# Optimization experiments

Hardware: AMD Instinct MI355X
Metric: run time of the kernel (lower is better)

## Reference

```python
import jax, jax.numpy as jnp
import numpy as np
from jax import lax

B, C_IN, C_OUT, H, W, K, MID = 16, 256, 256, 64, 64, 3, 64
BN_EPS = 1e-5


def setup_inputs() -> dict:
    key = jax.random.key(0)
    ks = jax.random.split(key, 16)
    inp = {
        'x': jax.random.normal(ks[0], (B, C_IN, H, W), dtype=jnp.float32),
        # 4 kernel banks: (4, c2, c1//g, k, k)
        'weight': jax.random.normal(ks[1], (4, C_OUT, C_IN, K, K), dtype=jnp.float32) * 0.05,
        'gamma': jnp.ones((C_OUT,), jnp.float32),
        'beta': jnp.zeros((C_OUT,), jnp.float32),
    }
    # four attention branches: Linear(c, mid, bias=False) -> ReLU -> Linear(mid, 4, bias=True)
    names = ['s', 'c', 'f', 'w']
    for i, n in enumerate(names):
        inp[f'fc_{n}_w1'] = jax.random.normal(ks[2 + 3 * i], (MID, C_IN), dtype=jnp.float32) * 0.05
        inp[f'fc_{n}_w2'] = jax.random.normal(ks[3 + 3 * i], (4, MID), dtype=jnp.float32) * 0.05
        inp[f'fc_{n}_b2'] = jax.random.normal(ks[4 + 3 * i], (4,), dtype=jnp.float32) * 0.05
    return inp


def _branch(pooled, w1, w2, b2):
    # pooled: [B, C]; w1: [MID, C]; w2: [4, MID]
    h = jax.nn.relu(pooled @ w1.T)
    return jax.nn.softmax(h @ w2.T + b2, axis=1)  # [B, 4]


def reference(x, weight, gamma, beta,
              fc_s_w1, fc_s_w2, fc_s_b2,
              fc_c_w1, fc_c_w2, fc_c_b2,
              fc_f_w1, fc_f_w2, fc_f_b2,
              fc_w_w1, fc_w_w2, fc_w_b2):
    b = x.shape[0]
    pooled = jnp.mean(x, axis=(2, 3))  # GAP -> [B, C]
    alpha = (_branch(pooled, fc_s_w1, fc_s_w2, fc_s_b2)
             * _branch(pooled, fc_c_w1, fc_c_w2, fc_c_b2)
             * _branch(pooled, fc_f_w1, fc_f_w2, fc_f_b2)
             * _branch(pooled, fc_w_w1, fc_w_w2, fc_w_b2))  # [B, 4]
    # per-sample dynamic kernels: [B, out_c, in_c, k, k]
    dyn_w = jnp.einsum('bn,noikl->boikl', alpha, weight)

    def conv_one(xi, wi):
        # xi: [C, H, W]; wi: [out_c, in_c, k, k]
        return lax.conv_general_dilated(
            xi[None], wi, window_strides=(1, 1), padding='SAME',
            dimension_numbers=('NCHW', 'OIHW', 'NCHW'))[0]

    out = jax.vmap(conv_one)(x, dyn_w)  # [B, out_c, H, W]

    # BatchNorm2d (training-mode batch statistics)
    mean = jnp.mean(out, axis=(0, 2, 3))
    var = jnp.var(out, axis=(0, 2, 3))
    out = (out - mean[None, :, None, None]) * jax.lax.rsqrt(var + BN_EPS)[None, :, None, None]
    return out * gamma[None, :, None, None] + beta[None, :, None, None]
```

## Files before the change

### kernel.cpp

```cpp
#include <hip/hip_runtime.h>
#include <math.h>

#define BB 16
#define CIN 256
#define COUT 256
#define HH 64
#define WW 64
#define NBANK_STRIDE 589824

typedef short bf16x8 __attribute__((ext_vector_type(8)));
typedef float f32x4 __attribute__((ext_vector_type(4)));

#define WS_XT_OFF 32768
#define WS_DW_OFF 33587200
#define WS_NEED   52461568ULL

static __device__ __forceinline__ short f2bf(float f) {
    union { float f; unsigned u; } v; v.f = f;
    unsigned r = v.u + 0x7FFF + ((v.u >> 16) & 1);
    return (short)(r >> 16);
}

struct AttnParams {
    const float* w1[4];
    const float* w2[4];
    const float* b2[4];
};

__global__ __launch_bounds__(256) void zero_kernel(float* __restrict__ ws) {
    ws[blockIdx.x * 256 + threadIdx.x] = 0.f;
}

__global__ __launch_bounds__(256) void xpose_kernel(const float* __restrict__ x,
                                                    short* __restrict__ xT,
                                                    float* __restrict__ pooled) {
    const int ci0 = blockIdx.x * 32;
    const int h = blockIdx.y;
    const int b = blockIdx.z;
    const int t = threadIdx.x;
    __shared__ __align__(16) short tile[64][40];
    {
        const int ci = t >> 3;
        const int l = t & 7;
        const float4* src = (const float4*)(x + ((size_t)(b * 256 + ci0 + ci)) * 4096 + h * 64);
        float4 v1 = src[l * 2];
        float4 v2 = src[l * 2 + 1];
        tile[l * 8 + 0][ci] = f2bf(v1.x);
        tile[l * 8 + 1][ci] = f2bf(v1.y);
        tile[l * 8 + 2][ci] = f2bf(v1.z);
        tile[l * 8 + 3][ci] = f2bf(v1.w);
        tile[l * 8 + 4][ci] = f2bf(v2.x);
        tile[l * 8 + 5][ci] = f2bf(v2.y);
        tile[l * 8 + 6][ci] = f2bf(v2.z);
        tile[l * 8 + 7][ci] = f2bf(v2.w);
        float s = v1.x + v1.y + v1.z + v1.w + v2.x + v2.y + v2.z + v2.w;
        s += __shfl_xor(s, 1, 64);
        s += __shfl_xor(s, 2, 64);
        s += __shfl_xor(s, 4, 64);
        if (l == 0) atomicAdd(&pooled[b * 256 + ci0 + ci], s);
    }
    __syncthreads();
    {
        const int w = t >> 2;
        const int s = t & 3;
        bf16x8 val = *(const bf16x8*)&tile[w][s * 8];
        *(bf16x8*)&xT[((size_t)b * 4096 + h * 64 + w) * 256 + ci0 + s * 8] = val;
    }
}

__global__ __launch_bounds__(256) void attn_kernel(AttnParams p, float* __restrict__ ws_f) {
    const int b = blockIdx.x;
    const int t = threadIdx.x;
    const int wv = t >> 6;
    const int lane = t & 63;
    __shared__ float ps[256];
    __shared__ float hs[4][64];
    __shared__ float lg[4][4];
    __shared__ float sm[4][4];
    ws_f[4096 + b * 256 + t] = 0.f;
    ps[t] = ws_f[b * 256 + t] * (1.0f / 4096.0f);
    __syncthreads();
    {
        const float4* w1v = (const float4*)(p.w1[wv] + lane * 256);
        float h = 0.f;
#pragma unroll 8
        for (int i = 0; i < 64; ++i) {
            float4 w4 = w1v[i];
            h += w4.x * ps[i * 4 + 0] + w4.y * ps[i * 4 + 1] +
                 w4.z * ps[i * 4 + 2] + w4.w * ps[i * 4 + 3];
        }
        hs[wv][lane] = fmaxf(h, 0.f);
    }
    __syncthreads();
    if (t < 16) {
        const int n = t >> 2, j = t & 3;
        const float* w2 = p.w2[n];
        float l = p.b2[n][j];
        for (int m = 0; m < 64; ++m) l += w2[j * 64 + m] * hs[n][m];
        lg[n][j] = l;
    }
    __syncthreads();
    if (t < 4) {
        const int n = t;
        float mx = fmaxf(fmaxf(lg[n][0], lg[n][1]), fmaxf(lg[n][2], lg[n][3]));
        float e0 = expf(lg[n][0] - mx), e1 = expf(lg[n][1] - mx);
        float e2 = expf(lg[n][2] - mx), e3 = expf(lg[n][3] - mx);
        float inv = 1.f / (e0 + e1 + e2 + e3);
        sm[n][0] = e0 * inv; sm[n][1] = e1 * inv; sm[n][2] = e2 * inv; sm[n][3] = e3 * inv;
    }
    __syncthreads();
    if (t < 4) ws_f[b * 256 + t] = sm[0][t] * sm[1][t] * sm[2][t] * sm[3][t];
}

__global__ __launch_bounds__(256) void dynw_kernel(const float* __restrict__ wt,
                                                   const float* __restrict__ ws_f,
                                                   short* __restrict__ dynwF) {
    const int co = blockIdx.x;
    const int ci = threadIdx.x;
    const int cotile = co >> 4;
    const int mh = co & 15;
    const int cc = ci >> 5;
    const int q = (ci >> 3) & 3;
    const int j = ci & 7;
    const int lane = q * 16 + mh;
    float w[4][9];
#pragma unroll
    for (int n = 0; n < 4; ++n) {
        const size_t base = ((size_t)(n * 256 + co) * 256 + ci) * 9;
#pragma unroll
        for (int k = 0; k < 9; ++k) w[n][k] = wt[base + k];
    }
    for (int b = 0; b < BB; ++b) {
        const float a0 = ws_f[b * 256 + 0];
        const float a1 = ws_f[b * 256 + 1];
        const float a2 = ws_f[b * 256 + 2];
        const float a3 = ws_f[b * 256 + 3];
#pragma unroll
        for (int k = 0; k < 9; ++k) {
            float v = a0 * w[0][k] + a1 * w[1][k] + a2 * w[2][k] + a3 * w[3][k];
            dynwF[(((((size_t)(b * 9 + k) * 16 + cotile) * 8 + cc) * 64 + lane) << 3) + j] = f2bf(v);
        }
    }
}

__global__ __launch_bounds__(256, 2) void conv_mfma_kernel(const short* __restrict__ xT,
                                                           const short* __restrict__ dynwF,
                                                           float* __restrict__ out,
                                                           float* __restrict__ bn_part) {
    const int id = blockIdx.x;
    const int xcd = id & 7;
    const int wi = id >> 3;
    const int b = xcd + ((wi >> 5) << 3);
    const int rem = wi & 31;
    const int mt = rem >> 4;
    const int nt = rem & 15;

    const int t = threadIdx.x;
    const int lane = t & 63;
    const int wv = t >> 6;
    const int wx = wv & 1;
    const int wy = wv >> 1;
    const int mh = lane & 15;
    const int q = lane >> 4;
    const int r0 = nt * 4;
    const int co0 = mt * 128;

    __shared__ __align__(16) short xs[396 * 64];
    __shared__ float red[128][2][2];

    f32x4 acc[4][8];
#pragma unroll
    for (int i = 0; i < 4; ++i)
#pragma unroll
        for (int j = 0; j < 8; ++j) acc[i][j] = (f32x4){0.f, 0.f, 0.f, 0.f};

    const short* Aw = dynwF + (size_t)b * 9 * 65536 + (mt * 8 + wy * 4) * 4096 + lane * 8;

    bf16x8 afn[4];
#pragma unroll
    for (int mi = 0; mi < 4; ++mi)
        afn[mi] = *(const bf16x8*)(Aw + mi * 4096);

    const bf16x8 zero8 = {0, 0, 0, 0, 0, 0, 0, 0};

    for (int cc = 0; cc < 8; ++cc) {
        const int ci0 = cc * 32;
        __syncthreads();
#pragma unroll
        for (int i = 0; i < 7; ++i) {
            int idx = t + 256 * i;
            if (idx < 1584) {
                int p = idx >> 2;
                int sub = idx & 3;
                int lr = p / 66;
                int lc = p - lr * 66;
                int r = r0 - 1 + lr;
                int c = lc - 1;
                bf16x8 v = zero8;
                if ((unsigned)r < 64u && (unsigned)c < 64u)
                    v = *(const bf16x8*)&xT[((size_t)b * 4096 + r * 64 + c) * 256 + ci0 + sub * 8];
                *(bf16x8*)&xs[(p << 6) + ((sub ^ (p & 7)) << 3)] = v;
            }
        }
        __syncthreads();
#pragma unroll
        for (int khw = 0; khw < 9; ++khw) {
            const int kh = khw / 3;
            const int kw = khw - kh * 3;
            bf16x8 af[4];
#pragma unroll
            for (int mi = 0; mi < 4; ++mi) af[mi] = afn[mi];
            {
                const int nkhw = (khw < 8) ? (khw + 1) : 0;
                const int ncc = (khw < 8) ? cc : ((cc < 7) ? cc + 1 : 7);
#pragma unroll
                for (int mi = 0; mi < 4; ++mi)
                    afn[mi] = *(const bf16x8*)(Aw + (size_t)nkhw * 65536 + mi * 4096 + ncc * 512);
            }
            bf16x8 bfr[8];
#pragma unroll
            for (int ni = 0; ni < 8; ++ni) {
                const int row_l = wx * 2 + (ni >> 2) + kh;
                const int col_l = (ni & 3) * 16 + kw + mh;
                const int pp = row_l * 66 + col_l;
                bfr[ni] = *(const bf16x8*)&xs[(pp << 6) + ((q ^ (pp & 7)) << 3)];
            }
#pragma unroll
            for (int mi = 0; mi < 4; ++mi)
#pragma unroll
                for (int ni = 0; ni < 8; ++ni)
                    acc[mi][ni] = __builtin_amdgcn_mfma_f32_16x16x32_bf16(af[mi], bfr[ni], acc[mi][ni], 0, 0, 0);
        }
    }

    float s16[4][4], q16[4][4];
#pragma unroll
    for (int mi = 0; mi < 4; ++mi)
#pragma unroll
        for (int reg = 0; reg < 4; ++reg) { s16[mi][reg] = 0.f; q16[mi][reg] = 0.f; }

#pragma unroll
    for (int mi = 0; mi < 4; ++mi) {
#pragma unroll
        for (int ni = 0; ni < 8; ++ni) {
            const int pix = wx * 128 + ni * 16 + mh;
            const int h = r0 + (pix >> 6);
            const int w = pix & 63;
#pragma unroll
            for (int reg = 0; reg < 4; ++reg) {
                const int co = co0 + wy * 64 + mi * 16 + q * 4 + reg;
                const float e = acc[mi][ni][reg];
                out[(((size_t)b * 256 + co) << 12) + (h << 6) + w] = e;
                s16[mi][reg] += e;
                q16[mi][reg] += e * e;
            }
        }
    }
#pragma unroll
    for (int mi = 0; mi < 4; ++mi)
#pragma unroll
        for (int reg = 0; reg < 4; ++reg) {
            float s = s16[mi][reg], sq = q16[mi][reg];
            s += __shfl_xor(s, 1, 64);  sq += __shfl_xor(sq, 1, 64);
            s += __shfl_xor(s, 2, 64);  sq += __shfl_xor(sq, 2, 64);
            s += __shfl_xor(s, 4, 64);  sq += __shfl_xor(sq, 4, 64);
            s += __shfl_xor(s, 8, 64);  sq += __shfl_xor(sq, 8, 64);
            if (mh == 0) {
                const int co_l = wy * 64 + mi * 16 + q * 4 + reg;
                red[co_l][0][wx] = s;
                red[co_l][1][wx] = sq;
            }
        }
    __syncthreads();
    {
        const int co_l = t >> 1;
        const int st = t & 1;
        float v = red[co_l][st][0] + red[co_l][st][1];
        atomicAdd(&bn_part[(st * 256 + co0 + co_l) * 8 + (nt & 7)], v);
    }
}

__global__ __launch_bounds__(256) void bn_finalize_kernel(const float* __restrict__ bn_part,
                                                          const float* __restrict__ gamma,
                                                          const float* __restrict__ beta,
                                                          float* __restrict__ scale,
                                                          float* __restrict__ shift) {
    const int co = threadIdx.x;
    float S = 0.f, Q = 0.f;
#pragma unroll
    for (int s = 0; s < 8; ++s) {
        S += bn_part[(co) * 8 + s];
        Q += bn_part[(256 + co) * 8 + s];
    }
    const float mean = S * (1.f / 65536.f);
    const float var = Q * (1.f / 65536.f) - mean * mean;
    const float inv = rsqrtf(var + 1e-5f);
    const float sc = gamma[co] * inv;
    scale[co] = sc;
    shift[co] = beta[co] - mean * sc;
}

__global__ __launch_bounds__(256) void bn_apply_kernel(float* __restrict__ out,
                                                       const float* __restrict__ scale,
                                                       const float* __restrict__ shift) {
    const int gid = blockIdx.x * 256 + threadIdx.x;
    const int c = (gid >> 10) & 255;
    float4* p = (float4*)out;
    float4 v = p[gid];
    const float sc = scale[c], sh = shift[c];
    v.x = v.x * sc + sh;
    v.y = v.y * sc + sh;
    v.z = v.z * sc + sh;
    v.w = v.w * sc + sh;
    p[gid] = v;
}

__global__ __launch_bounds__(256) void gap_kernel(const float* __restrict__ x,
                                                  float* __restrict__ pooled) {
    const int plane = blockIdx.x;
    const float4* p = (const float4*)(x + (size_t)plane * 4096);
    const int t = threadIdx.x;
    float s = 0.f;
#pragma unroll
    for (int i = 0; i < 4; ++i) {
        float4 v = p[t + 256 * i];
        s += v.x + v.y + v.z + v.w;
    }
#pragma unroll
    for (int off = 32; off > 0; off >>= 1) s += __shfl_down(s, off, 64);
    __shared__ float red[4];
    if ((t & 63) == 0) red[t >> 6] = s;
    __syncthreads();
    if (t == 0) pooled[plane] = (red[0] + red[1] + red[2] + red[3]) * (1.0f / 4096.0f);
}

__global__ __launch_bounds__(64) void attn64_kernel(const float* __restrict__ pooled,
                                                    AttnParams p,
                                                    float* __restrict__ alpha) {
    const int b = blockIdx.x;
    const int t = threadIdx.x;
    __shared__ float ps[256];
    __shared__ float hs[64];
    __shared__ float lg[4];
    __shared__ float prod[4];
#pragma unroll
    for (int i = 0; i < 4; ++i) ps[t + 64 * i] = pooled[b * 256 + t + 64 * i];
    if (t < 4) prod[t] = 1.f;
    __syncthreads();
    for (int n = 0; n < 4; ++n) {
        const float* w1 = p.w1[n];
        float h = 0.f;
        for (int c = 0; c < 256; ++c) h += w1[t * 256 + c] * ps[c];
        hs[t] = fmaxf(h, 0.f);
        __syncthreads();
        if (t < 4) {
            const float* w2 = p.w2[n];
            float l = p.b2[n][t];
            for (int m = 0; m < 64; ++m) l += w2[t * 64 + m] * hs[m];
            lg[t] = l;
        }
        __syncthreads();
        if (t == 0) {
            float mx = fmaxf(fmaxf(lg[0], lg[1]), fmaxf(lg[2], lg[3]));
            float e0 = expf(lg[0] - mx), e1 = expf(lg[1] - mx);
            float e2 = expf(lg[2] - mx), e3 = expf(lg[3] - mx);
            float inv = 1.f / (e0 + e1 + e2 + e3);
            prod[0] *= e0 * inv; prod[1] *= e1 * inv;
            prod[2] *= e2 * inv; prod[3] *= e3 * inv;
        }
        __syncthreads();
    }
    if (t < 4) alpha[b * 4 + t] = prod[t];
}

__global__ __launch_bounds__(256) void conv_fp32_kernel(const float* __restrict__ x,
                                                        const float* __restrict__ wt,
                                                        const float* __restrict__ alpha,
                                                        float* __restrict__ out) {
    const int h = blockIdx.x;
    const int cot = blockIdx.y;
    const int b = blockIdx.z;
    const int t = threadIdx.x;
    const int tx = t & 15;
    const int ty = t >> 4;
    const int co0 = cot * 64;
    __shared__ __align__(16) float xsf[32][68];
    __shared__ __align__(16) float wshf[3][32][68];
    const float a0 = alpha[b * 4 + 0], a1 = alpha[b * 4 + 1];
    const float a2 = alpha[b * 4 + 2], a3 = alpha[b * 4 + 3];
    float acc[4][4];
#pragma unroll
    for (int i = 0; i < 4; ++i)
#pragma unroll
        for (int j = 0; j < 4; ++j) acc[i][j] = 0.f;
    const size_t xbase = (size_t)b * CIN * 4096;
    for (int kh = 0; kh < 3; ++kh) {
        const int r = h + kh - 1;
        if (r < 0 || r >= HH) continue;
        for (int chunk = 0; chunk < 8; ++chunk) {
            const int ci0 = chunk * 32;
            __syncthreads();
#pragma unroll
            for (int i = 0; i < 8; ++i) {
                int flat = t + 256 * i;
                int ci = flat >> 6;
                int w = flat & 63;
                xsf[ci][1 + w] = x[xbase + (size_t)(ci0 + ci) * 4096 + r * 64 + w];
            }
            if (t < 32) { xsf[t][0] = 0.f; xsf[t][65] = 0.f; xsf[t][66] = 0.f; xsf[t][67] = 0.f; }
#pragma unroll
            for (int j = 0; j < 24; ++j) {
                int e = t + 256 * j;
                int co = e / 96;
                int rem = e - co * 96;
                int ci = rem / 3;
                int kw = rem - ci * 3;
                size_t g = (((size_t)(co0 + co) * 256 + (ci0 + ci)) * 3 + kh) * 3 + kw;
                wshf[kw][ci][co] = a0 * wt[g] + a1 * wt[g + NBANK_STRIDE] +
                                   a2 * wt[g + 2 * NBANK_STRIDE] + a3 * wt[g + 3 * NBANK_STRIDE];
            }
            __syncthreads();
            for (int ci = 0; ci < 32; ++ci) {
                float4 w0 = *(const float4*)&wshf[0][ci][tx * 4];
                float4 w1v = *(const float4*)&wshf[1][ci][tx * 4];
                float4 w2v = *(const float4*)&wshf[2][ci][tx * 4];
                float4 xa = *(const float4*)&xsf[ci][ty * 4];
                float4 xb = *(const float4*)&xsf[ci][ty * 4 + 4];
                float v[8] = {xa.x, xa.y, xa.z, xa.w, xb.x, xb.y, xb.z, xb.w};
                float aw[3][4] = {{w0.x, w0.y, w0.z, w0.w},
                                  {w1v.x, w1v.y, w1v.z, w1v.w},
                                  {w2v.x, w2v.y, w2v.z, w2v.w}};
#pragma unroll
                for (int kw = 0; kw < 3; ++kw)
#pragma unroll
                    for (int i = 0; i < 4; ++i)
#pragma unroll
                        for (int j = 0; j < 4; ++j)
                            acc[i][j] += aw[kw][i] * v[j + kw];
            }
        }
    }
    size_t obase = (((size_t)b * COUT + co0 + tx * 4) * 64 + h) * 64 + ty * 4;
#pragma unroll
    for (int i = 0; i < 4; ++i) {
        float4 o = {acc[i][0], acc[i][1], acc[i][2], acc[i][3]};
        *(float4*)&out[obase + (size_t)i * 4096] = o;
    }
}

__global__ __launch_bounds__(256) void bn_stats_kernel(const float* __restrict__ out,
                                                       const float* __restrict__ gamma,
                                                       const float* __restrict__ beta,
                                                       float* __restrict__ scale,
                                                       float* __restrict__ shift) {
    const int co = blockIdx.x;
    const int t = threadIdx.x;
    float s = 0.f, sq = 0.f;
    for (int b = 0; b < BB; ++b) {
        const float4* p = (const float4*)(out + ((size_t)b * 256 + co) * 4096);
#pragma unroll
        for (int i = 0; i < 4; ++i) {
            float4 v = p[t + 256 * i];
            s += v.x + v.y + v.z + v.w;
            sq += v.x * v.x + v.y * v.y + v.z * v.z + v.w * v.w;
        }
    }
#pragma unroll
    for (int off = 32; off > 0; off >>= 1) {
        s += __shfl_down(s, off, 64);
        sq += __shfl_down(sq, off, 64);
    }
    __shared__ float rs[4], rq[4];
    if ((t & 63) == 0) { rs[t >> 6] = s; rq[t >> 6] = sq; }
    __syncthreads();
    if (t == 0) {
        float S = rs[0] + rs[1] + rs[2] + rs[3];
        float Q = rq[0] + rq[1] + rq[2] + rq[3];
        float mean = S * (1.f / 65536.f);
        float var = Q * (1.f / 65536.f) - mean * mean;
        float inv = rsqrtf(var + 1e-5f);
        float sc = gamma[co] * inv;
        scale[co] = sc;
        shift[co] = beta[co] - mean * sc;
    }
}

extern "C" void kernel_launch(void* const* d_in, const int* in_sizes, int n_in,
                              void* d_out, int out_size, void* d_ws, size_t ws_size,
                              hipStream_t stream) {
    (void)in_sizes; (void)n_in; (void)out_size;
    const float* x = (const float*)d_in[0];
    const float* wt = (const float*)d_in[1];
    const float* gamma = (const float*)d_in[2];
    const float* beta = (const float*)d_in[3];
    AttnParams ap;
    for (int n = 0; n < 4; ++n) {
        ap.w1[n] = (const float*)d_in[4 + 3 * n];
        ap.w2[n] = (const float*)d_in[5 + 3 * n];
        ap.b2[n] = (const float*)d_in[6 + 3 * n];
    }
    float* ws_f = (float*)d_ws;
    float* out = (float*)d_out;

    if (ws_size >= WS_NEED) {
        short* xT = (short*)((char*)d_ws + WS_XT_OFF);
        short* dynwF = (short*)((char*)d_ws + WS_DW_OFF);
        float* bn_part = ws_f + 4096;
        float* scale = ws_f;
        float* shift = ws_f + 256;

        zero_kernel<<<16, 256, 0, stream>>>(ws_f);
        xpose_kernel<<<dim3(8, 64, 16), 256, 0, stream>>>(x, xT, ws_f);
        attn_kernel<<<16, 256, 0, stream>>>(ap, ws_f);
        dynw_kernel<<<256, 256, 0, stream>>>(wt, ws_f, dynwF);
        conv_mfma_kernel<<<512, 256, 0, stream>>>(xT, dynwF, out, bn_part);
        bn_finalize_kernel<<<1, 256, 0, stream>>>(bn_part, gamma, beta, scale, shift);
        bn_apply_kernel<<<16384, 256, 0, stream>>>(out, scale, shift);
    } else {
        float* pooled = ws_f;
        float* alpha = ws_f + 4096;
        float* scale = ws_f + 4160;
        float* shift = ws_f + 4416;
        gap_kernel<<<4096, 256, 0, stream>>>(x, pooled);
        attn64_kernel<<<16, 64, 0, stream>>>(pooled, ap, alpha);
        conv_fp32_kernel<<<dim3(64, 4, 16), 256, 0, stream>>>(x, wt, alpha, out);
        bn_stats_kernel<<<256, 256, 0, stream>>>(out, gamma, beta, scale, shift);
        bn_apply_kernel<<<16384, 256, 0, stream>>>(out, scale, shift);
    }
}
```

Before: 323.2 us.

## Stage dynamic-weight A fragments through LDS with async global_load_lds triple buffer

Replaces direct per-lane global register prefetch of the dynamic weight fragments with asynchronous global_load_lds copies into a three-slot LDS ring, issued two kh/kw steps ahead. A vmcnt wait plus a workgroup barrier after each MFMA step keeps the slots consistent. The goal is to hide global latency and free VGPRs. In exchange it adds a barrier per inner iteration and more LDS use, which may lower occupancy.

```diff
diff --git a/kernel.cpp b/kernel.cpp
--- a/kernel.cpp
+++ b/kernel.cpp
@@ -166,6 +166,7 @@
     const int co0 = mt * 128;
 
     __shared__ __align__(16) short xs[396 * 64];
+    __shared__ __align__(16) short As[2][3][2048];
     __shared__ float red[128][2][2];
 
     f32x4 acc[4][8];
@@ -174,12 +175,22 @@
 #pragma unroll
         for (int j = 0; j < 8; ++j) acc[i][j] = (f32x4){0.f, 0.f, 0.f, 0.f};
 
-    const short* Aw = dynwF + (size_t)b * 9 * 65536 + (mt * 8 + wy * 4) * 4096 + lane * 8;
-
-    bf16x8 afn[4];
-#pragma unroll
-    for (int mi = 0; mi < 4; ++mi)
-        afn[mi] = *(const bf16x8*)(Aw + mi * 4096);
+    const size_t a_b9 = (size_t)b * 9;
+    const int a_cot0 = mt * 8 + wy * 4;
+
+    auto stage_A = [&](int k, int cc_, int par_) {
+#pragma unroll
+        for (int ci_t = 0; ci_t < 4; ++ci_t) {
+            const short* src = dynwF + (((((a_b9 + k) * 16 + a_cot0 + ci_t) * 8 + cc_) * 64 + lane) << 3);
+            __builtin_amdgcn_global_load_lds(
+                (const __attribute__((address_space(1))) void*)src,
+                (__attribute__((address_space(3))) void*)&As[wy][par_][ci_t * 512],
+                16, 0, 0);
+        }
+    };
+
+    stage_A(0, 0, 0);
+    stage_A(1, 0, 1);
 
     const bf16x8 zero8 = {0, 0, 0, 0, 0, 0, 0, 0};
 
@@ -207,16 +218,13 @@
         for (int khw = 0; khw < 9; ++khw) {
             const int kh = khw / 3;
             const int kw = khw - kh * 3;
+            const int par = khw % 3;
+
             bf16x8 af[4];
 #pragma unroll
-            for (int mi = 0; mi < 4; ++mi) af[mi] = afn[mi];
-            {
-                const int nkhw = (khw < 8) ? (khw + 1) : 0;
-                const int ncc = (khw < 8) ? cc : ((cc < 7) ? cc + 1 : 7);
-#pragma unroll
-                for (int mi = 0; mi < 4; ++mi)
-                    afn[mi] = *(const bf16x8*)(Aw + (size_t)nkhw * 65536 + mi * 4096 + ncc * 512);
-            }
+            for (int mi = 0; mi < 4; ++mi)
+                af[mi] = *(const bf16x8*)&As[wy][par][mi * 512 + lane * 8];
+
             bf16x8 bfr[8];
 #pragma unroll
             for (int ni = 0; ni < 8; ++ni) {
@@ -225,11 +233,23 @@
                 const int pp = row_l * 66 + col_l;
                 bfr[ni] = *(const bf16x8*)&xs[(pp << 6) + ((q ^ (pp & 7)) << 3)];
             }
+
+            if (!(cc == 7 && khw >= 7)) {
+                const int nkh = (khw < 7) ? (khw + 2) : (khw - 7);
+                const int ncc = (khw < 7) ? cc : (cc + 1);
+                stage_A(nkh, ncc, (khw + 2) % 3);
+            }
+
 #pragma unroll
             for (int mi = 0; mi < 4; ++mi)
 #pragma unroll
                 for (int ni = 0; ni < 8; ++ni)
                     acc[mi][ni] = __builtin_amdgcn_mfma_f32_16x16x32_bf16(af[mi], bfr[ni], acc[mi][ni], 0, 0, 0);
+
+            asm volatile("s_waitcnt vmcnt(4)" ::: "memory");
+            __builtin_amdgcn_sched_barrier(0);
+            __builtin_amdgcn_s_barrier();
+            __builtin_amdgcn_sched_barrier(0);
         }
     }
 
```

Result: slower. 399.8 us (+23.7%).

## Stage dynamic-weight A tiles through double-buffered LDS instead of per-wave global loads

Applied to the files above, without the earlier changes.

Each workgroup now loads the per-sample weight slice for a kernel tap cooperatively, with every thread fetching 32 bytes, and stores it in a double-buffered LDS array. Waves then read their A fragments from LDS rather than each wave loading its own fragments directly from global memory. The aim is to cut redundant global/L2 traffic, since waves sharing the same rows no longer fetch them separately. In exchange it adds a __syncthreads per tap (9 per channel chunk), 16KB of extra LDS that may lower occupancy, and LDS reads on the MFMA critical path.

```diff
diff --git a/kernel.cpp b/kernel.cpp
--- a/kernel.cpp
+++ b/kernel.cpp
@@ -166,6 +166,7 @@
     const int co0 = mt * 128;
 
     __shared__ __align__(16) short xs[396 * 64];
+    __shared__ __align__(16) short As[2][4096];
     __shared__ float red[128][2][2];
 
     f32x4 acc[4][8];
@@ -174,18 +175,20 @@
 #pragma unroll
         for (int j = 0; j < 8; ++j) acc[i][j] = (f32x4){0.f, 0.f, 0.f, 0.f};
 
-    const short* Aw = dynwF + (size_t)b * 9 * 65536 + (mt * 8 + wy * 4) * 4096 + lane * 8;
-
-    bf16x8 afn[4];
-#pragma unroll
-    for (int mi = 0; mi < 4; ++mi)
-        afn[mi] = *(const bf16x8*)(Aw + mi * 4096);
+    const size_t a_b9 = (size_t)b * 9;
+    const int a_ct = mt * 8 + (t >> 5);
+    const int a_port16 = (t & 31) * 16;
+    const int a_dst = (t >> 5) * 512 + a_port16;
+    const int a_rd0 = (wy * 4) * 512 + lane * 8;
 
     const bf16x8 zero8 = {0, 0, 0, 0, 0, 0, 0, 0};
 
     for (int cc = 0; cc < 8; ++cc) {
         const int ci0 = cc * 32;
         __syncthreads();
+        const short* asrc0 = dynwF + ((((a_b9 + 0) * 16 + a_ct) * 8 + cc) << 9) + a_port16;
+        bf16x8 pa0 = *(const bf16x8*)(asrc0);
+        bf16x8 pa1 = *(const bf16x8*)(asrc0 + 8);
 #pragma unroll
         for (int i = 0; i < 7; ++i) {
             int idx = t + 256 * i;
@@ -202,20 +205,18 @@
                 *(bf16x8*)&xs[(p << 6) + ((sub ^ (p & 7)) << 3)] = v;
             }
         }
+        *(bf16x8*)&As[0][a_dst] = pa0;
+        *(bf16x8*)&As[0][a_dst + 8] = pa1;
         __syncthreads();
 #pragma unroll
         for (int khw = 0; khw < 9; ++khw) {
             const int kh = khw / 3;
             const int kw = khw - kh * 3;
-            bf16x8 af[4];
-#pragma unroll
-            for (int mi = 0; mi < 4; ++mi) af[mi] = afn[mi];
-            {
-                const int nkhw = (khw < 8) ? (khw + 1) : 0;
-                const int ncc = (khw < 8) ? cc : ((cc < 7) ? cc + 1 : 7);
-#pragma unroll
-                for (int mi = 0; mi < 4; ++mi)
-                    afn[mi] = *(const bf16x8*)(Aw + (size_t)nkhw * 65536 + mi * 4096 + ncc * 512);
+            bf16x8 na0, na1;
+            if (khw < 8) {
+                const short* s = dynwF + ((((a_b9 + khw + 1) * 16 + a_ct) * 8 + cc) << 9) + a_port16;
+                na0 = *(const bf16x8*)(s);
+                na1 = *(const bf16x8*)(s + 8);
             }
             bf16x8 bfr[8];
 #pragma unroll
@@ -226,10 +227,17 @@
                 bfr[ni] = *(const bf16x8*)&xs[(pp << 6) + ((q ^ (pp & 7)) << 3)];
             }
 #pragma unroll
-            for (int mi = 0; mi < 4; ++mi)
+            for (int mi = 0; mi < 4; ++mi) {
+                bf16x8 af = *(const bf16x8*)&As[khw & 1][a_rd0 + mi * 512];
 #pragma unroll
                 for (int ni = 0; ni < 8; ++ni)
-                    acc[mi][ni] = __builtin_amdgcn_mfma_f32_16x16x32_bf16(af[mi], bfr[ni], acc[mi][ni], 0, 0, 0);
+                    acc[mi][ni] = __builtin_amdgcn_mfma_f32_16x16x32_bf16(af, bfr[ni], acc[mi][ni], 0, 0, 0);
+            }
+            if (khw < 8) {
+                *(bf16x8*)&As[(khw + 1) & 1][a_dst] = na0;
+                *(bf16x8*)&As[(khw + 1) & 1][a_dst + 8] = na1;
+                __syncthreads();
+            }
         }
     }
 
```

Result: faster. 274.3 us (-15.1%).
